# Kernel tuning notes

Measured on AMD Instinct MI355X. Metric: run time of the kernel, lower is better.

## Reference

```python
import jax, jax.numpy as jnp
import numpy as np

T, WQ, WS, C, H, W = 2, 75, 25, 640, 10, 10
WAY, SHOT = 5, 5
HID = C // 16
SCALE_VALUE = 30.0
ATTEN_SCALE_VALUE = 50.0
FROM_VALUE = 0.5
VALUE_INTERVAL = 0.3
BN_EPS = 1e-5
NORM_EPS = 1e-12


def _leaky(x):
    return jnp.where(x >= 0, x, 0.2 * x)


def _l2norm(x, axis):
    n = jnp.sqrt(jnp.sum(x * x, axis=axis, keepdims=True))
    return x / jnp.maximum(n, NORM_EPS)


def _embed(x, W_conv, bn_gamma, bn_beta, bn_mean, bn_var):
    # 1x1 conv (no bias) + eval-mode BatchNorm + LeakyReLU(0.2)
    # x: [t, n, c, h, w] -> [t, n, c, h, w]
    y = jnp.einsum('oc,tnchw->tnohw', W_conv, x)
    inv = bn_gamma / jnp.sqrt(bn_var + BN_EPS)
    y = y * inv[:, None, None] + (bn_beta - bn_mean * inv)[:, None, None]
    return _leaky(y)


def setup_inputs() -> dict:
    key = jax.random.key(0)
    ks = jax.random.split(key, 5)
    return {
        'query_feat': jax.random.normal(ks[0], (T, WQ, C, H, W), dtype=jnp.float32),
        'support_feat': jax.random.normal(ks[1], (T, WS, C, H, W), dtype=jnp.float32),
        'W_conv': jax.random.normal(ks[2], (C, C), dtype=jnp.float32) * 0.02,
        'bn_gamma': jnp.ones((C,), jnp.float32),
        'bn_beta': jnp.zeros((C,), jnp.float32),
        'bn_mean': jnp.zeros((C,), jnp.float32),
        'bn_var': jnp.ones((C,), jnp.float32),
        'psi_w1': jax.random.normal(ks[3], (C, HID), dtype=jnp.float32) * 0.04,
        'psi_b1': jnp.zeros((HID,), jnp.float32),
        'psi_w2': jax.random.normal(ks[4], (HID, 1), dtype=jnp.float32) * 0.15,
        'psi_b2': jnp.zeros((1,), jnp.float32),
        'way_num': WAY,
        'shot_num': SHOT,
    }


def reference(query_feat, support_feat, W_conv, bn_gamma, bn_beta, bn_mean, bn_var,
              psi_w1, psi_b1, psi_w2, psi_b2, way_num, shot_num):
    t, wq, c, h, w = query_feat.shape
    ws = support_feat.shape[1]
    hw = h * w

    # embedded + normalized features for the gated branch
    w_query = _embed(query_feat, W_conv, bn_gamma, bn_beta, bn_mean, bn_var)
    w_query = w_query.reshape(t, wq, c, hw).transpose(0, 1, 3, 2)      # [t, wq, hw, c]
    w_support = _embed(support_feat, W_conv, bn_gamma, bn_beta, bn_mean, bn_var)
    w_support = w_support.reshape(t, ws, c, hw).transpose(0, 2, 1, 3).reshape(t, c, ws * hw)
    w_query = _l2norm(w_query, axis=3)
    w_support = _l2norm(w_support, axis=1)

    # cosine similarity of embedded features: [t, wq, hw, ws*hw]
    f_x = jnp.einsum('tqpc,tck->tqpk', w_query, w_support)

    # AEAModule: per-location adaptive threshold from f_psi MLP
    hid = _leaky(w_query @ psi_w1 + psi_b1)                            # [t, wq, hw, HID]
    clamp_value = jax.nn.sigmoid(hid @ psi_w2 + psi_b2) * VALUE_INTERVAL + FROM_VALUE
    clamp_fx = jax.nn.sigmoid(ATTEN_SCALE_VALUE * (f_x - clamp_value))
    atten_score = clamp_fx / jnp.maximum(
        jnp.sum(jnp.abs(clamp_fx), axis=-1, keepdims=True), NORM_EPS)  # L1 normalize

    # raw-feature cosine similarity
    qf = _l2norm(query_feat.reshape(t, wq, c, hw).transpose(0, 1, 3, 2), axis=3)
    sf = _l2norm(support_feat.reshape(t, ws, c, hw).transpose(0, 2, 1, 3).reshape(t, c, ws * hw), axis=1)
    match_score = jnp.einsum('tqpc,tck->tqpk', qf, sf)                 # [t, wq, hw, ws*hw]

    # gate, regroup support axis into (way, shot, hw_s), reduce
    ams = (atten_score * match_score).reshape(t, wq, hw, way_num, shot_num, hw)
    score = ams.sum(axis=-1).mean(axis=(2, 4)) * SCALE_VALUE           # [t, wq, way]
    return score
```

## Files before the change

### kernel.cpp

```cpp
#include <hip/hip_runtime.h>
#include <stdint.h>

#define T_    2
#define WQ_   75
#define WS_   25
#define C_    640
#define HW_   100
#define HID_  40
#define WAY_  5
#define QP_   (WQ_*HW_)
#define SP_   (WS_*HW_)
#define QPAD_ 128
#define KPAD_ 512
#define KROWS_ (WAY_*KPAD_)
#define C8_   (C_/8)
#define BM_   256
#define QSTR_ (C8_*QPAD_*8)

typedef _Float16 f16;
typedef _Float16 f16x8 __attribute__((ext_vector_type(8)));
typedef _Float16 f16x4 __attribute__((ext_vector_type(4)));
typedef _Float16 f16x16 __attribute__((ext_vector_type(16)));
typedef float    f32x4 __attribute__((ext_vector_type(4)));
typedef float    f32x16 __attribute__((ext_vector_type(16)));
typedef uint32_t u32;

__device__ __forceinline__ void gl_lds16(const f16* g, f16* l) {
  __builtin_amdgcn_global_load_lds(
      (const __attribute__((address_space(1))) u32*)g,
      (__attribute__((address_space(3))) u32*)l, 16, 0, 0);
}

__global__ __launch_bounds__(128) void k0_invnorm(
    const float* __restrict__ q, const float* __restrict__ s,
    float* __restrict__ rq_inv, float* __restrict__ rq_nrm,
    float* __restrict__ rs_inv, float* __restrict__ rs_nrm) {
  int b = blockIdx.x;
  int t = b / (WQ_ + WS_);
  int n = b % (WQ_ + WS_);
  int p = threadIdx.x;
  if (p >= HW_) return;
  const float* base; float* oi; float* on; int idx;
  if (n < WQ_) {
    base = q + ((size_t)(t*WQ_ + n))*C_*HW_;
    idx = t*QP_ + n*HW_ + p; oi = rq_inv; on = rq_nrm;
  } else {
    int m = n - WQ_;
    base = s + ((size_t)(t*WS_ + m))*C_*HW_;
    idx = t*SP_ + m*HW_ + p; oi = rs_inv; on = rs_nrm;
  }
  float ss = 0.f;
  for (int c = 0; c < C_; ++c) { float v = base[c*HW_ + p]; ss += v*v; }
  float nrm = fmaxf(sqrtf(ss), 1e-12f);
  oi[idx] = 1.f/nrm; on[idx] = nrm;
}

__global__ __launch_bounds__(256) void kw_packW(
    const float* __restrict__ W, const float* __restrict__ w1,
    f16* __restrict__ Wr, f16* __restrict__ Wt8, f16* __restrict__ w1t) {
  int idx = blockIdx.x*256 + threadIdx.x;
  if (idx < C_*C8_) {
    int o = idx / C8_, c8 = idx % C8_;
    f16x8 v;
#pragma unroll
    for (int i = 0; i < 8; ++i) v[i] = (f16)W[(size_t)o*C_ + c8*8 + i];
    *reinterpret_cast<f16x8*>(Wr + (size_t)o*C_ + c8*8) = v;
    *reinterpret_cast<f16x8*>(Wt8 + ((size_t)c8*C_ + o)*8) = v;
  } else if (idx < C_*C8_ + 48*C8_) {
    int k2 = idx - C_*C8_;
    int h = k2 / C8_, c8 = k2 % C8_;
    f16x8 v;
#pragma unroll
    for (int i = 0; i < 8; ++i)
      v[i] = (h < HID_) ? (f16)w1[(size_t)(c8*8+i)*HID_ + h] : (f16)0.f;
    *reinterpret_cast<f16x8*>(w1t + (size_t)h*C_ + c8*8) = v;
  }
}

__global__ __launch_bounds__(256) void k1_pack_qraw(
    const float* __restrict__ q, const float* __restrict__ rq_inv,
    f16* __restrict__ Bq_raw) {
  int b = blockIdx.x;
  int ct = b % 10; b /= 10;
  int qq = b % WQ_; int t = b / WQ_;
  int c0 = ct*64;
  size_t tq = (size_t)t*WQ_ + qq;
  __shared__ float lds[64*HW_];
  const float4* s4 = reinterpret_cast<const float4*>(
      q + ((tq)*C_ + c0)*HW_);
  float4* l4 = reinterpret_cast<float4*>(lds);
  for (int i = threadIdx.x; i < 64*HW_/4; i += 256) l4[i] = s4[i];
  __syncthreads();
  for (int ch = threadIdx.x; ch < 8*QPAD_; ch += 256) {
    int lc8 = ch / QPAD_, p = ch % QPAD_;
    float inv = (p < HW_) ? rq_inv[t*QP_ + qq*HW_ + p] : 0.f;
    f16x8 v;
#pragma unroll
    for (int i = 0; i < 8; ++i) {
      float x = (p < HW_) ? lds[(lc8*8 + i)*HW_ + p] : 0.f;
      v[i] = (f16)(x * inv);
    }
    *reinterpret_cast<f16x8*>(Bq_raw + (tq*C8_ + c0/8 + lc8)*((size_t)QPAD_*8) + (size_t)p*8) = v;
  }
}

__global__ __launch_bounds__(256) void k2_pack_sraw(
    const float* __restrict__ s, const float* __restrict__ rs_inv,
    f16* __restrict__ As_raw) {
  int b = blockIdx.x;
  int ct = b % 10; b /= 10;
  int n = b % WS_; int t = b / WS_;
  int c0 = ct*64;
  __shared__ float lds[64*HW_];
  const float4* s4 = reinterpret_cast<const float4*>(
      s + (((size_t)(t*WS_ + n))*C_ + c0)*HW_);
  float4* l4 = reinterpret_cast<float4*>(lds);
  for (int i = threadIdx.x; i < 64*HW_/4; i += 256) l4[i] = s4[i];
  __syncthreads();
  for (int ch = threadIdx.x; ch < HW_*8; ch += 256) {
    int p = ch / 8, cc = ch % 8;
    float inv = rs_inv[t*SP_ + n*HW_ + p];
    f16x8 v;
#pragma unroll
    for (int i = 0; i < 8; ++i) v[i] = (f16)(lds[(cc*8 + i)*HW_ + p] * inv);
    int k = n*HW_ + p;
    int way = k / 500, ki = k % 500;
    size_t row = (size_t)t*KROWS_ + way*KPAD_ + ki;
    *reinterpret_cast<f16x8*>(As_raw + row*C_ + c0 + cc*8) = v;
  }
}

__global__ __launch_bounds__(512) void k3_embed_support(
    const f16* __restrict__ As_raw, const f16* __restrict__ Wt8,
    const float* __restrict__ rs_nrm,
    const float* __restrict__ g, const float* __restrict__ be,
    const float* __restrict__ mu, const float* __restrict__ va,
    f16* __restrict__ As_emb) {
  int b = blockIdx.x;
  int t = b / (KROWS_/64);
  int row0 = (b % (KROWS_/64)) * 64;
  int tid = threadIdx.x, wv = tid >> 6, lane = tid & 63;
  int mf = wv & 3, nh = wv >> 2;
  __shared__ f16 Alds[64*32];
  __shared__ f16 Blds[32*C_];
  __shared__ float rowss[64];
  f32x4 acc[20];
#pragma unroll
  for (int i = 0; i < 20; ++i) acc[i] = (f32x4){0.f,0.f,0.f,0.f};

  for (int cs = 0; cs < 20; ++cs) {
    int c0 = cs*32;
    if (tid < 256) {
      int r = tid >> 2, ch = tid & 3;
      *reinterpret_cast<f16x8*>(Alds + r*32 + ch*8) =
        *reinterpret_cast<const f16x8*>(As_raw + ((size_t)t*KROWS_ + row0 + r)*C_ + c0 + ch*8);
    }
    const f16x8* bsrc = reinterpret_cast<const f16x8*>(Wt8 + (size_t)(c0/8)*C_*8);
    f16x8* bdst = reinterpret_cast<f16x8*>(Blds);
    for (int i = tid; i < 4*C_; i += 512) bdst[i] = bsrc[i];
    __syncthreads();
    f16x8 a = *reinterpret_cast<const f16x8*>(Alds + (mf*16 + (lane&15))*32 + (lane>>4)*8);
#pragma unroll
    for (int nf = 0; nf < 20; ++nf) {
      int o = nh*320 + nf*16 + (lane & 15);
      f16x8 bf = *reinterpret_cast<const f16x8*>(Blds + (((lane>>4)*C_) + o)*8);
      acc[nf] = __builtin_amdgcn_mfma_f32_16x16x32_f16(a, bf, acc[nf], 0, 0, 0);
    }
    __syncthreads();
  }

  if (tid < 64) rowss[tid] = 0.f;
  __syncthreads();
  int rg = lane >> 4, cl = lane & 15;
  int prow = row0 + mf*16 + rg*4;
#pragma unroll
  for (int j = 0; j < 4; ++j) {
    int pr = prow + j;
    int way = pr / KPAD_, ki = pr - way*KPAD_;
    bool valid = ki < 500;
    float nrm = valid ? rs_nrm[t*SP_ + way*500 + ki] : 0.f;
    float ssum = 0.f;
#pragma unroll
    for (int nf = 0; nf < 20; ++nf) {
      int o = nh*320 + nf*16 + cl;
      float inv = g[o] / sqrtf(va[o] + 1e-5f);
      float sh = be[o] - mu[o]*inv;
      float y = acc[nf][j]*nrm*inv + sh;
      y = (y >= 0.f) ? y : 0.2f*y;
      if (!valid) y = 0.f;
      acc[nf][j] = y;
      ssum += y*y;
    }
#pragma unroll
    for (int m = 1; m < 16; m <<= 1) ssum += __shfl_xor(ssum, m);
    if (cl == 0) atomicAdd(&rowss[mf*16 + rg*4 + j], ssum);
  }
  __syncthreads();
#pragma unroll
  for (int j = 0; j < 4; ++j) {
    int pr = prow + j;
    int ki = pr - (pr / KPAD_)*KPAD_;
    if (ki >= 500) continue;
    float invn = 1.f / fmaxf(sqrtf(rowss[mf*16 + rg*4 + j]), 1e-12f);
#pragma unroll
    for (int nf = 0; nf < 20; ++nf) {
      int o = nh*320 + nf*16 + cl;
      As_emb[((size_t)t*KROWS_ + pr)*C_ + o] = (f16)(acc[nf][j]*invn);
    }
  }
}

__global__ __launch_bounds__(256, 3) void k4_embed_query(
    const f16* __restrict__ Wr, const f16* __restrict__ Bq_raw,
    const float* __restrict__ rq_nrm,
    const float* __restrict__ g, const float* __restrict__ be,
    const float* __restrict__ mu, const float* __restrict__ va,
    f16* __restrict__ Bq_emb) {
  __shared__ f16 Ab[3][128*32];
  __shared__ f16 Bb[3][4*QPAD_*8];
  int b = blockIdx.x;
  int ot = b % 5; b /= 5;
  int qq = b % WQ_; int t = b / WQ_;
  int o0 = ot*128;
  size_t tq = (size_t)t*WQ_ + qq;
  int tid = threadIdx.x, w = tid >> 6, lane = tid & 63;
  int la_r = lane >> 2, la_c = lane & 3;

  auto stage = [&](int buf, int cs) {
#pragma unroll
    for (int i = 0; i < 2; ++i) {
      int ca = w*2 + i;
      int r = ca*16 + la_r;
      int sc = la_c ^ (r & 3);
      gl_lds16(Wr + (size_t)(o0 + r)*C_ + cs*32 + sc*8, &Ab[buf][ca*512]);
    }
#pragma unroll
    for (int i = 0; i < 2; ++i) {
      int cb = w*2 + i;
      int c8l = cb >> 1;
      size_t src = (tq*C8_ + cs*4 + c8l)*(size_t)(QPAD_*8) + (size_t)((cb&1)*64 + lane)*8;
      gl_lds16(Bq_raw + src, &Bb[buf][(c8l*QPAD_ + (cb&1)*64)*8]);
    }
  };

  f32x4 acc[2][8];
#pragma unroll
  for (int a = 0; a < 2; ++a)
#pragma unroll
    for (int n = 0; n < 8; ++n) acc[a][n] = (f32x4){0.f,0.f,0.f,0.f};

  stage(0, 0);
  stage(1, 1);
  for (int cs = 0; cs < 20; ++cs) {
    int buf = cs % 3;
    if (cs < 19) asm volatile("s_waitcnt vmcnt(4)" ::: "memory");
    else         asm volatile("s_waitcnt vmcnt(0)" ::: "memory");
    __builtin_amdgcn_s_barrier();
    if (cs < 18) stage((cs+2)%3, cs+2);
    __builtin_amdgcn_s_setprio(1);
    f16x8 fa[2];
#pragma unroll
    for (int mi = 0; mi < 2; ++mi) {
      int R = w*32 + mi*16 + (lane & 15);
      int sc = (lane >> 4) ^ (R & 3);
      fa[mi] = *reinterpret_cast<const f16x8*>(&Ab[buf][R*32 + sc*8]);
    }
#pragma unroll
    for (int nf = 0; nf < 8; ++nf) {
      f16x8 fb = *reinterpret_cast<const f16x8*>(
          &Bb[buf][((lane>>4)*QPAD_ + nf*16 + (lane&15))*8]);
#pragma unroll
      for (int mi = 0; mi < 2; ++mi)
        acc[mi][nf] = __builtin_amdgcn_mfma_f32_16x16x32_f16(fa[mi], fb, acc[mi][nf], 0, 0, 0);
    }
    __builtin_amdgcn_s_setprio(0);
  }

#pragma unroll
  for (int mi = 0; mi < 2; ++mi) {
    int obase = o0 + w*32 + mi*16 + (lane>>4)*4;
    float inv4[4], sh4[4];
#pragma unroll
    for (int j = 0; j < 4; ++j) {
      int o = obase + j;
      inv4[j] = g[o] / sqrtf(va[o] + 1e-5f);
      sh4[j] = be[o] - mu[o]*inv4[j];
    }
#pragma unroll
    for (int nf = 0; nf < 8; ++nf) {
      int pp = nf*16 + (lane & 15);
      float nrmv = (pp < HW_) ? rq_nrm[t*QP_ + qq*HW_ + pp] : 0.f;
      f16x4 vv;
#pragma unroll
      for (int j = 0; j < 4; ++j) {
        float y = (pp < HW_) ? (acc[mi][nf][j]*nrmv*inv4[j] + sh4[j]) : 0.f;
        y = (y >= 0.f) ? y : 0.2f*y;
        vv[j] = (f16)y;
      }
      *reinterpret_cast<f16x4*>(
          &Bq_emb[(tq*C8_ + (obase>>3))*((size_t)QPAD_*8) + (size_t)pp*8 + (obase&7)]) = vv;
    }
  }
}

__global__ __launch_bounds__(256) void k5_colnorm_psi(
    f16* __restrict__ Bq_emb, const f16* __restrict__ w1t,
    const float* __restrict__ b1, const float* __restrict__ w2,
    const float* __restrict__ b2, float* __restrict__ cv) {
  __shared__ float ssA[2][QPAD_];
  __shared__ float invs[QPAD_];
  __shared__ float hidL[48*QPAD_];
  int bq = blockIdx.x;
  int tid = threadIdx.x, w = tid >> 6, lane = tid & 63;
  size_t base = (size_t)bq * QSTR_;

  {
    int h2 = tid >> 7, pp = tid & 127;
    float ss = 0.f;
    for (int c8 = h2*40; c8 < h2*40 + 40; ++c8) {
      f16x8 v = *reinterpret_cast<const f16x8*>(&Bq_emb[base + ((size_t)c8*QPAD_ + pp)*8]);
#pragma unroll
      for (int i = 0; i < 8; ++i) { float x = (float)v[i]; ss += x*x; }
    }
    ssA[h2][pp] = ss;
  }
  for (int i = tid; i < 48*QPAD_; i += 256) hidL[i] = 0.f;
  __syncthreads();
  if (tid < QPAD_) invs[tid] = 1.f / fmaxf(sqrtf(ssA[0][tid] + ssA[1][tid]), 1e-12f);

  f32x4 acc[3][8];
#pragma unroll
  for (int a = 0; a < 3; ++a)
#pragma unroll
    for (int n = 0; n < 8; ++n) acc[a][n] = (f32x4){0.f,0.f,0.f,0.f};
  for (int r = 0; r < 5; ++r) {
    int cs = w + r*4;
    f16x8 fa[3];
#pragma unroll
    for (int mf = 0; mf < 3; ++mf) {
      int R = mf*16 + (lane & 15);
      fa[mf] = *reinterpret_cast<const f16x8*>(&w1t[(size_t)R*C_ + cs*32 + (lane>>4)*8]);
    }
#pragma unroll
    for (int nf = 0; nf < 8; ++nf) {
      f16x8 fb = *reinterpret_cast<const f16x8*>(
          &Bq_emb[base + ((size_t)(cs*4 + (lane>>4))*QPAD_ + nf*16 + (lane&15))*8]);
#pragma unroll
      for (int mf = 0; mf < 3; ++mf)
        acc[mf][nf] = __builtin_amdgcn_mfma_f32_16x16x32_f16(fa[mf], fb, acc[mf][nf], 0, 0, 0);
    }
  }
  __syncthreads();
  for (int rr = 0; rr < 4; ++rr) {
    if (w == rr) {
#pragma unroll
      for (int mf = 0; mf < 3; ++mf)
#pragma unroll
        for (int nf = 0; nf < 8; ++nf)
#pragma unroll
          for (int j = 0; j < 4; ++j) {
            int row = mf*16 + (lane>>4)*4 + j;
            int col = nf*16 + (lane & 15);
            hidL[row*QPAD_ + col] += acc[mf][nf][j];
          }
    }
    __syncthreads();
  }
  if (tid < QPAD_) {
    float inv = invs[tid];
    float z = b2[0];
    for (int h = 0; h < HID_; ++h) {
      float hv = hidL[h*QPAD_ + tid]*inv + b1[h];
      hv = (hv >= 0.f) ? hv : 0.2f*hv;
      z += hv*w2[h];
    }
    cv[bq*QPAD_ + tid] = 0.3f/(1.f + __expf(-z)) + 0.5f;
  }
  for (int i = tid; i < C8_*QPAD_; i += 256) {
    int pp = i & 127;
    f16* ptr = Bq_emb + base + (size_t)i*8;
    f16x8 v = *reinterpret_cast<const f16x8*>(ptr);
    float inv = invs[pp];
    f16x8 o;
#pragma unroll
    for (int j = 0; j < 8; ++j) o[j] = (f16)((float)v[j]*inv);
    *reinterpret_cast<f16x8*>(ptr) = o;
  }
}

__global__ __launch_bounds__(256, 2) void k6_main(
    const f16* __restrict__ As_emb, const f16* __restrict__ As_raw,
    const f16* __restrict__ Bq_emb, const f16* __restrict__ Bq_raw,
    const float* __restrict__ cv,
    float* __restrict__ Spart, float* __restrict__ L1part) {
  __shared__ f16 Ab[3][BM_*32];
  __shared__ f16 Bb[3][4*QPAD_*8];
  __shared__ float cvs[QPAD_], Ss[QPAD_], L1s[QPAD_];

  int bid = blockIdx.x;
  int xcd = bid & 7, j0 = bid >> 3;
  int l = (xcd < 4) ? xcd*188 + j0 : 752 + (xcd-4)*187 + j0;
  int kt = l & 1; int m = l >> 1;
  int q = m % WQ_; int gidx = m / WQ_;
  int t = gidx / WAY_, way = gidx - t*WAY_;

  int tid = threadIdx.x, w = tid >> 6, lane = tid & 63;
  size_t tq = (size_t)t*WQ_ + q;
  if (tid < QPAD_) {
    cvs[tid] = cv[tq*QPAD_ + tid];
    Ss[tid] = 0.f; L1s[tid] = 0.f;
  }
  int wrow0 = w*64;
  int la_r = lane >> 2, la_c = lane & 3;
  size_t Arowbase = (size_t)t*KROWS_ + (size_t)way*KPAD_ + (size_t)kt*BM_;

  auto stage = [&](int buf, int ph) {
    int pass = ph / 20, cs = ph - pass*20;
    const f16* As = (pass == 0) ? As_raw : As_emb;
    const f16* Bs = (pass == 0) ? Bq_raw : Bq_emb;
#pragma unroll
    for (int i = 0; i < 4; ++i) {
      int ca = w*4 + i;
      int r = ca*16 + la_r;
      int sc = la_c ^ (r & 3);
      gl_lds16(As + (Arowbase + r)*C_ + cs*32 + sc*8, &Ab[buf][ca*512]);
    }
#pragma unroll
    for (int i = 0; i < 2; ++i) {
      int cb = w*2 + i;
      int c8l = cb >> 1;
      size_t src = (tq*C8_ + cs*4 + c8l)*(size_t)(QPAD_*8) + (size_t)((cb&1)*64 + lane)*8;
      gl_lds16(Bs + src, &Bb[buf][(c8l*QPAD_ + (cb&1)*64)*8]);
    }
  };

  f32x16 acc[2][4];
  f16x16 mtc[2][4];
#pragma unroll
  for (int mi = 0; mi < 2; ++mi)
#pragma unroll
    for (int nf = 0; nf < 4; ++nf) acc[mi][nf] = (f32x16)(0.f);
  float Sl[4] = {0,0,0,0}, L1l[4] = {0,0,0,0};

  stage(0, 0);
  stage(1, 1);

  for (int ph = 0; ph < 40; ++ph) {
    int buf = ph % 3;
    if (ph < 39) asm volatile("s_waitcnt vmcnt(6)" ::: "memory");
    else         asm volatile("s_waitcnt vmcnt(0)" ::: "memory");
    __builtin_amdgcn_s_barrier();
    if (ph < 38) stage((ph+2)%3, ph+2);
    __builtin_amdgcn_s_setprio(1);
    const f16* Abuf = Ab[buf];
    const f16* Bbuf = Bb[buf];
    int r0 = wrow0 + (lane & 31);
    int r1 = r0 + 32;
    int rsw = r0 & 3;
#pragma unroll
    for (int ks = 0; ks < 2; ++ks) {
      int c8l = ks*2 + (lane >> 5);
      int pc = c8l ^ rsw;
      f16x8 fa0 = *reinterpret_cast<const f16x8*>(&Abuf[r0*32 + pc*8]);
      f16x8 fa1 = *reinterpret_cast<const f16x8*>(&Abuf[r1*32 + pc*8]);
#pragma unroll
      for (int nf = 0; nf < 4; ++nf) {
        f16x8 fb = *reinterpret_cast<const f16x8*>(
            &Bbuf[(c8l*QPAD_ + nf*32 + (lane & 31))*8]);
        acc[0][nf] = __builtin_amdgcn_mfma_f32_32x32x16_f16(fa0, fb, acc[0][nf], 0, 0, 0);
        acc[1][nf] = __builtin_amdgcn_mfma_f32_32x32x16_f16(fa1, fb, acc[1][nf], 0, 0, 0);
      }
    }
    __builtin_amdgcn_s_setprio(0);

    if (ph == 19) {
#pragma unroll
      for (int mi = 0; mi < 2; ++mi)
#pragma unroll
        for (int nf = 0; nf < 4; ++nf) {
#pragma unroll
          for (int jj = 0; jj < 16; ++jj) {
            mtc[mi][nf][jj] = (f16)acc[mi][nf][jj];
            acc[mi][nf][jj] = 0.f;
          }
        }
    } else if (ph == 39) {
#pragma unroll
      for (int mi = 0; mi < 2; ++mi)
#pragma unroll
        for (int nf = 0; nf < 4; ++nf) {
          float cvv = cvs[nf*32 + (lane & 31)];
#pragma unroll
          for (int jj = 0; jj < 16; ++jj) {
            float sg = 1.f/(1.f + __expf(-50.f*(acc[mi][nf][jj] - cvv)));
            Sl[nf]  += sg * (float)mtc[mi][nf][jj];
            L1l[nf] += sg;
          }
        }
    }
  }

#pragma unroll
  for (int nf = 0; nf < 4; ++nf) {
    float vs = Sl[nf] + __shfl_xor(Sl[nf], 32);
    float vl = L1l[nf] + __shfl_xor(L1l[nf], 32);
    if (lane < 32) {
      atomicAdd(&Ss[nf*32 + lane], vs);
      atomicAdd(&L1s[nf*32 + lane], vl);
    }
  }
  __syncthreads();
  if (tid < QPAD_) {
    size_t o = ((tq*WAY_ + way)*2 + kt)*(size_t)QPAD_ + tid;
    Spart[o] = Ss[tid]; L1part[o] = L1s[tid];
  }
}

__global__ __launch_bounds__(128) void k7_reduce(
    const float* __restrict__ Spart, const float* __restrict__ L1part,
    float* __restrict__ out) {
  int b = blockIdx.x;
  int tid = threadIdx.x;
  __shared__ float red[128];
  float contrib[WAY_] = {0,0,0,0,0};
  if (tid < HW_) {
    size_t base = (size_t)b*WAY_*2*QPAD_;
    float l1 = 0.f;
#pragma unroll
    for (int w = 0; w < WAY_; ++w)
#pragma unroll
      for (int k = 0; k < 2; ++k) l1 += L1part[base + (w*2+k)*QPAD_ + tid];
    l1 = fmaxf(l1, 1e-12f);
#pragma unroll
    for (int w = 0; w < WAY_; ++w)
      contrib[w] = (Spart[base + (w*2+0)*QPAD_ + tid] +
                    Spart[base + (w*2+1)*QPAD_ + tid]) / l1;
  }
#pragma unroll
  for (int w = 0; w < WAY_; ++w) {
    red[tid] = contrib[w];
    __syncthreads();
    for (int off = 64; off > 0; off >>= 1) {
      if (tid < off) red[tid] += red[tid + off];
      __syncthreads();
    }
    if (tid == 0) out[b*WAY_ + w] = red[0] * 30.f / (float)(HW_*5);
    __syncthreads();
  }
}

extern "C" void kernel_launch(void* const* d_in, const int* in_sizes, int n_in,
                              void* d_out, int out_size, void* d_ws, size_t ws_size,
                              hipStream_t stream) {
  (void)in_sizes; (void)n_in; (void)out_size; (void)ws_size;
  const float* q  = (const float*)d_in[0];
  const float* s  = (const float*)d_in[1];
  const float* W  = (const float*)d_in[2];
  const float* g  = (const float*)d_in[3];
  const float* be = (const float*)d_in[4];
  const float* mu = (const float*)d_in[5];
  const float* va = (const float*)d_in[6];
  const float* w1 = (const float*)d_in[7];
  const float* b1 = (const float*)d_in[8];
  const float* w2 = (const float*)d_in[9];
  const float* b2 = (const float*)d_in[10];
  float* out = (float*)d_out;
  char* ws = (char*)d_ws;

  size_t off = 0;
  auto nxt = [&](size_t bytes) { size_t o = off; off += (bytes + 255) & ~(size_t)255; return o; };
  float* rq_inv = (float*)(ws + nxt((size_t)T_*QP_*4));
  float* rq_nrm = (float*)(ws + nxt((size_t)T_*QP_*4));
  float* rs_inv = (float*)(ws + nxt((size_t)T_*SP_*4));
  float* rs_nrm = (float*)(ws + nxt((size_t)T_*SP_*4));
  f16* Wr     = (f16*)(ws + nxt((size_t)C_*C_*2));
  f16* Wt8    = (f16*)(ws + nxt((size_t)C_*C_*2));
  f16* w1t    = (f16*)(ws + nxt((size_t)48*C_*2));
  f16* As_raw = (f16*)(ws + nxt((size_t)T_*KROWS_*C_*2));
  f16* As_emb = (f16*)(ws + nxt((size_t)T_*KROWS_*C_*2));
  f16* Bq_raw = (f16*)(ws + nxt((size_t)T_*WQ_*QSTR_*2));
  f16* Bq_emb = (f16*)(ws + nxt((size_t)T_*WQ_*QSTR_*2));
  float* cvp    = (float*)(ws + nxt((size_t)T_*WQ_*QPAD_*4));
  float* Spart  = (float*)(ws + nxt((size_t)T_*WQ_*WAY_*2*QPAD_*4));
  float* L1part = (float*)(ws + nxt((size_t)T_*WQ_*WAY_*2*QPAD_*4));

  hipMemsetAsync(As_raw, 0, (size_t)T_*KROWS_*C_*2, stream);
  hipMemsetAsync(As_emb, 0, (size_t)T_*KROWS_*C_*2, stream);

  k0_invnorm<<<T_*(WQ_+WS_), 128, 0, stream>>>(q, s, rq_inv, rq_nrm, rs_inv, rs_nrm);
  kw_packW<<<(C_*C8_ + 48*C8_ + 255)/256, 256, 0, stream>>>(W, w1, Wr, Wt8, w1t);
  k1_pack_qraw<<<T_*WQ_*10, 256, 0, stream>>>(q, rq_inv, Bq_raw);
  k2_pack_sraw<<<T_*WS_*10, 256, 0, stream>>>(s, rs_inv, As_raw);
  k3_embed_support<<<T_*(KROWS_/64), 512, 0, stream>>>(As_raw, Wt8, rs_nrm, g, be, mu, va, As_emb);
  k4_embed_query<<<T_*WQ_*5, 256, 0, stream>>>(Wr, Bq_raw, rq_nrm, g, be, mu, va, Bq_emb);
  k5_colnorm_psi<<<T_*WQ_, 256, 0, stream>>>(Bq_emb, w1t, b1, w2, b2, cvp);
  k6_main<<<1500, 256, 0, stream>>>(As_emb, As_raw, Bq_emb, Bq_raw, cvp, Spart, L1part);
  k7_reduce<<<T_*WQ_, 128, 0, stream>>>(Spart, L1part, out);
}
```

Before: 337.3 us.

## Re-layout support matrices channel-blocked, defer query normalization, split k0 reduction

The support raw and embedded matrices are stored channel-group-major ([c8][row][8]), so each k6 stage becomes a few contiguous 16-byte global-to-LDS loads with simple pointer increments instead of swizzled per-row loads. The in-place rescale pass over Bq_emb in k5 is dropped; the per-query inverse norm is stored and applied to the accumulator inside k6's epilogue. k0 now spreads its channel reduction over 512 threads with an LDS combine. The match-score f16 cache is clamped to [-8, 8] before conversion, and the unswizzled LDS layout may add bank conflicts.

```diff
diff --git a/kernel.cpp b/kernel.cpp
--- a/kernel.cpp
+++ b/kernel.cpp
@@ -31,15 +31,16 @@
       (__attribute__((address_space(3))) u32*)l, 16, 0, 0);
 }
 
-__global__ __launch_bounds__(128) void k0_invnorm(
+__global__ __launch_bounds__(512) void k0_invnorm(
     const float* __restrict__ q, const float* __restrict__ s,
     float* __restrict__ rq_inv, float* __restrict__ rq_nrm,
     float* __restrict__ rs_inv, float* __restrict__ rs_nrm) {
+  __shared__ float part[4][128];
   int b = blockIdx.x;
   int t = b / (WQ_ + WS_);
   int n = b % (WQ_ + WS_);
-  int p = threadIdx.x;
-  if (p >= HW_) return;
+  int tid = threadIdx.x;
+  int seg = tid >> 7, p = tid & 127;
   const float* base; float* oi; float* on; int idx;
   if (n < WQ_) {
     base = q + ((size_t)(t*WQ_ + n))*C_*HW_;
@@ -50,9 +51,18 @@
     idx = t*SP_ + m*HW_ + p; oi = rs_inv; on = rs_nrm;
   }
   float ss = 0.f;
-  for (int c = 0; c < C_; ++c) { float v = base[c*HW_ + p]; ss += v*v; }
-  float nrm = fmaxf(sqrtf(ss), 1e-12f);
-  oi[idx] = 1.f/nrm; on[idx] = nrm;
+  if (p < HW_) {
+    for (int c = seg*160; c < seg*160 + 160; ++c) {
+      float v = base[c*HW_ + p]; ss += v*v;
+    }
+  }
+  part[seg][p] = ss;
+  __syncthreads();
+  if (seg == 0 && p < HW_) {
+    float tot = part[0][p] + part[1][p] + part[2][p] + part[3][p];
+    float nrm = fmaxf(sqrtf(tot), 1e-12f);
+    oi[idx] = 1.f/nrm; on[idx] = nrm;
+  }
 }
 
 __global__ __launch_bounds__(256) void kw_packW(
@@ -125,8 +135,8 @@
     for (int i = 0; i < 8; ++i) v[i] = (f16)(lds[(cc*8 + i)*HW_ + p] * inv);
     int k = n*HW_ + p;
     int way = k / 500, ki = k % 500;
-    size_t row = (size_t)t*KROWS_ + way*KPAD_ + ki;
-    *reinterpret_cast<f16x8*>(As_raw + row*C_ + c0 + cc*8) = v;
+    size_t row = (size_t)way*KPAD_ + ki;
+    *reinterpret_cast<f16x8*>(As_raw + ((size_t)(t*C8_ + c0/8 + cc)*KROWS_ + row)*8) = v;
   }
 }
 
@@ -149,17 +159,18 @@
   for (int i = 0; i < 20; ++i) acc[i] = (f32x4){0.f,0.f,0.f,0.f};
 
   for (int cs = 0; cs < 20; ++cs) {
-    int c0 = cs*32;
     if (tid < 256) {
-      int r = tid >> 2, ch = tid & 3;
-      *reinterpret_cast<f16x8*>(Alds + r*32 + ch*8) =
-        *reinterpret_cast<const f16x8*>(As_raw + ((size_t)t*KROWS_ + row0 + r)*C_ + c0 + ch*8);
-    }
-    const f16x8* bsrc = reinterpret_cast<const f16x8*>(Wt8 + (size_t)(c0/8)*C_*8);
+      int c8l = tid >> 6, r = tid & 63;
+      *reinterpret_cast<f16x8*>(Alds + (c8l*64 + r)*8) =
+        *reinterpret_cast<const f16x8*>(
+            As_raw + ((size_t)(t*C8_ + cs*4 + c8l)*KROWS_ + row0 + r)*8);
+    }
+    const f16x8* bsrc = reinterpret_cast<const f16x8*>(Wt8 + (size_t)(cs*4)*C_*8);
     f16x8* bdst = reinterpret_cast<f16x8*>(Blds);
     for (int i = tid; i < 4*C_; i += 512) bdst[i] = bsrc[i];
     __syncthreads();
-    f16x8 a = *reinterpret_cast<const f16x8*>(Alds + (mf*16 + (lane&15))*32 + (lane>>4)*8);
+    f16x8 a = *reinterpret_cast<const f16x8*>(
+        Alds + ((lane>>4)*64 + mf*16 + (lane&15))*8);
 #pragma unroll
     for (int nf = 0; nf < 20; ++nf) {
       int o = nh*320 + nf*16 + (lane & 15);
@@ -205,7 +216,7 @@
 #pragma unroll
     for (int nf = 0; nf < 20; ++nf) {
       int o = nh*320 + nf*16 + cl;
-      As_emb[((size_t)t*KROWS_ + pr)*C_ + o] = (f16)(acc[nf][j]*invn);
+      As_emb[((size_t)(t*C8_ + (o>>3))*KROWS_ + pr)*8 + (o&7)] = (f16)(acc[nf][j]*invn);
     }
   }
 }
@@ -304,9 +315,10 @@
 }
 
 __global__ __launch_bounds__(256) void k5_colnorm_psi(
-    f16* __restrict__ Bq_emb, const f16* __restrict__ w1t,
+    const f16* __restrict__ Bq_emb, const f16* __restrict__ w1t,
     const float* __restrict__ b1, const float* __restrict__ w2,
-    const float* __restrict__ b2, float* __restrict__ cv) {
+    const float* __restrict__ b2, float* __restrict__ cv,
+    float* __restrict__ invq) {
   __shared__ float ssA[2][QPAD_];
   __shared__ float invs[QPAD_];
   __shared__ float hidL[48*QPAD_];
@@ -326,7 +338,12 @@
   }
   for (int i = tid; i < 48*QPAD_; i += 256) hidL[i] = 0.f;
   __syncthreads();
-  if (tid < QPAD_) invs[tid] = 1.f / fmaxf(sqrtf(ssA[0][tid] + ssA[1][tid]), 1e-12f);
+  if (tid < QPAD_) {
+    float ss = ssA[0][tid] + ssA[1][tid];
+    float inv = (ss > 0.f) ? (1.f / fmaxf(sqrtf(ss), 1e-12f)) : 0.f;
+    invs[tid] = inv;
+    invq[bq*QPAD_ + tid] = inv;
+  }
 
   f32x4 acc[3][8];
 #pragma unroll
@@ -376,26 +393,16 @@
     }
     cv[bq*QPAD_ + tid] = 0.3f/(1.f + __expf(-z)) + 0.5f;
   }
-  for (int i = tid; i < C8_*QPAD_; i += 256) {
-    int pp = i & 127;
-    f16* ptr = Bq_emb + base + (size_t)i*8;
-    f16x8 v = *reinterpret_cast<const f16x8*>(ptr);
-    float inv = invs[pp];
-    f16x8 o;
-#pragma unroll
-    for (int j = 0; j < 8; ++j) o[j] = (f16)((float)v[j]*inv);
-    *reinterpret_cast<f16x8*>(ptr) = o;
-  }
 }
 
 __global__ __launch_bounds__(256, 2) void k6_main(
     const f16* __restrict__ As_emb, const f16* __restrict__ As_raw,
     const f16* __restrict__ Bq_emb, const f16* __restrict__ Bq_raw,
-    const float* __restrict__ cv,
+    const float* __restrict__ cv, const float* __restrict__ invq,
     float* __restrict__ Spart, float* __restrict__ L1part) {
-  __shared__ f16 Ab[3][BM_*32];
+  __shared__ f16 Ab[3][4*BM_*8];
   __shared__ f16 Bb[3][4*QPAD_*8];
-  __shared__ float cvs[QPAD_], Ss[QPAD_], L1s[QPAD_];
+  __shared__ float cvs[QPAD_], iqs[QPAD_], Ss[QPAD_], L1s[QPAD_];
 
   int bid = blockIdx.x;
   int xcd = bid & 7, j0 = bid >> 3;
@@ -408,30 +415,30 @@
   size_t tq = (size_t)t*WQ_ + q;
   if (tid < QPAD_) {
     cvs[tid] = cv[tq*QPAD_ + tid];
+    iqs[tid] = invq[tq*QPAD_ + tid];
     Ss[tid] = 0.f; L1s[tid] = 0.f;
   }
   int wrow0 = w*64;
-  int la_r = lane >> 2, la_c = lane & 3;
-  size_t Arowbase = (size_t)t*KROWS_ + (size_t)way*KPAD_ + (size_t)kt*BM_;
-
-  auto stage = [&](int buf, int ph) {
-    int pass = ph / 20, cs = ph - pass*20;
-    const f16* As = (pass == 0) ? As_raw : As_emb;
-    const f16* Bs = (pass == 0) ? Bq_raw : Bq_emb;
-#pragma unroll
-    for (int i = 0; i < 4; ++i) {
-      int ca = w*4 + i;
-      int r = ca*16 + la_r;
-      int sc = la_c ^ (r & 3);
-      gl_lds16(As + (Arowbase + r)*C_ + cs*32 + sc*8, &Ab[buf][ca*512]);
-    }
-#pragma unroll
-    for (int i = 0; i < 2; ++i) {
-      int cb = w*2 + i;
-      int c8l = cb >> 1;
-      size_t src = (tq*C8_ + cs*4 + c8l)*(size_t)(QPAD_*8) + (size_t)((cb&1)*64 + lane)*8;
-      gl_lds16(Bs + src, &Bb[buf][(c8l*QPAD_ + (cb&1)*64)*8]);
-    }
+  size_t rowb = (size_t)way*KPAD_ + (size_t)kt*BM_;
+
+  const size_t aoff = ((size_t)(t*C8_ + w)*KROWS_ + rowb + lane)*8;
+  const size_t boff = ((tq*C8_ + w)*(size_t)QPAD_ + lane)*8;
+  const f16* pA = As_raw + aoff;
+  const f16* pB = Bq_raw + boff;
+  const f16* pA1 = As_emb + aoff;
+  const f16* pB1 = Bq_emb + boff;
+  const int CS_A = 4*KROWS_*8;
+  const int CS_B = 4*QPAD_*8;
+
+  auto stage = [&](int buf, const f16* a, const f16* bsrc) {
+    f16* da = &Ab[buf][(size_t)w*BM_*8];
+    f16* db = &Bb[buf][(size_t)w*QPAD_*8];
+    gl_lds16(a,        da);
+    gl_lds16(a + 512,  da + 512);
+    gl_lds16(a + 1024, da + 1024);
+    gl_lds16(a + 1536, da + 1536);
+    gl_lds16(bsrc,       db);
+    gl_lds16(bsrc + 512, db + 512);
   };
 
   f32x16 acc[2][4];
@@ -442,27 +449,25 @@
     for (int nf = 0; nf < 4; ++nf) acc[mi][nf] = (f32x16)(0.f);
   float Sl[4] = {0,0,0,0}, L1l[4] = {0,0,0,0};
 
-  stage(0, 0);
-  stage(1, 1);
+  stage(0, pA, pB); pA += CS_A; pB += CS_B;
+  stage(1, pA, pB); pA += CS_A; pB += CS_B;
 
   for (int ph = 0; ph < 40; ++ph) {
+    if (ph == 18) { pA = pA1; pB = pB1; }
     int buf = ph % 3;
     if (ph < 39) asm volatile("s_waitcnt vmcnt(6)" ::: "memory");
     else         asm volatile("s_waitcnt vmcnt(0)" ::: "memory");
     __builtin_amdgcn_s_barrier();
-    if (ph < 38) stage((ph+2)%3, ph+2);
+    if (ph < 38) { stage((ph+2)%3, pA, pB); pA += CS_A; pB += CS_B; }
     __builtin_amdgcn_s_setprio(1);
     const f16* Abuf = Ab[buf];
     const f16* Bbuf = Bb[buf];
     int r0 = wrow0 + (lane & 31);
-    int r1 = r0 + 32;
-    int rsw = r0 & 3;
 #pragma unroll
     for (int ks = 0; ks < 2; ++ks) {
       int c8l = ks*2 + (lane >> 5);
-      int pc = c8l ^ rsw;
-      f16x8 fa0 = *reinterpret_cast<const f16x8*>(&Abuf[r0*32 + pc*8]);
-      f16x8 fa1 = *reinterpret_cast<const f16x8*>(&Abuf[r1*32 + pc*8]);
+      f16x8 fa0 = *reinterpret_cast<const f16x8*>(&Abuf[(c8l*BM_ + r0)*8]);
+      f16x8 fa1 = *reinterpret_cast<const f16x8*>(&Abuf[(c8l*BM_ + r0 + 32)*8]);
 #pragma unroll
       for (int nf = 0; nf < 4; ++nf) {
         f16x8 fb = *reinterpret_cast<const f16x8*>(
@@ -480,23 +485,26 @@
         for (int nf = 0; nf < 4; ++nf) {
 #pragma unroll
           for (int jj = 0; jj < 16; ++jj) {
-            mtc[mi][nf][jj] = (f16)acc[mi][nf][jj];
+            mtc[mi][nf][jj] = (f16)fminf(fmaxf(acc[mi][nf][jj], -8.f), 8.f);
             acc[mi][nf][jj] = 0.f;
           }
         }
     } else if (ph == 39) {
 #pragma unroll
-      for (int mi = 0; mi < 2; ++mi)
-#pragma unroll
-        for (int nf = 0; nf < 4; ++nf) {
-          float cvv = cvs[nf*32 + (lane & 31)];
+      for (int nf = 0; nf < 4; ++nf) {
+        int col = nf*32 + (lane & 31);
+        float cvv = cvs[col];
+        float iq = iqs[col];
+#pragma unroll
+        for (int mi = 0; mi < 2; ++mi)
 #pragma unroll
           for (int jj = 0; jj < 16; ++jj) {
-            float sg = 1.f/(1.f + __expf(-50.f*(acc[mi][nf][jj] - cvv)));
+            float fx = acc[mi][nf][jj] * iq;
+            float sg = 1.f/(1.f + __expf(-50.f*(fx - cvv)));
             Sl[nf]  += sg * (float)mtc[mi][nf][jj];
             L1l[nf] += sg;
           }
-        }
+      }
     }
   }
 
@@ -581,19 +589,20 @@
   f16* Bq_raw = (f16*)(ws + nxt((size_t)T_*WQ_*QSTR_*2));
   f16* Bq_emb = (f16*)(ws + nxt((size_t)T_*WQ_*QSTR_*2));
   float* cvp    = (float*)(ws + nxt((size_t)T_*WQ_*QPAD_*4));
+  float* invq   = (float*)(ws + nxt((size_t)T_*WQ_*QPAD_*4));
   float* Spart  = (float*)(ws + nxt((size_t)T_*WQ_*WAY_*2*QPAD_*4));
   float* L1part = (float*)(ws + nxt((size_t)T_*WQ_*WAY_*2*QPAD_*4));
 
   hipMemsetAsync(As_raw, 0, (size_t)T_*KROWS_*C_*2, stream);
   hipMemsetAsync(As_emb, 0, (size_t)T_*KROWS_*C_*2, stream);
 
-  k0_invnorm<<<T_*(WQ_+WS_), 128, 0, stream>>>(q, s, rq_inv, rq_nrm, rs_inv, rs_nrm);
+  k0_invnorm<<<T_*(WQ_+WS_), 512, 0, stream>>>(q, s, rq_inv, rq_nrm, rs_inv, rs_nrm);
   kw_packW<<<(C_*C8_ + 48*C8_ + 255)/256, 256, 0, stream>>>(W, w1, Wr, Wt8, w1t);
   k1_pack_qraw<<<T_*WQ_*10, 256, 0, stream>>>(q, rq_inv, Bq_raw);
   k2_pack_sraw<<<T_*WS_*10, 256, 0, stream>>>(s, rs_inv, As_raw);
   k3_embed_support<<<T_*(KROWS_/64), 512, 0, stream>>>(As_raw, Wt8, rs_nrm, g, be, mu, va, As_emb);
   k4_embed_query<<<T_*WQ_*5, 256, 0, stream>>>(Wr, Bq_raw, rq_nrm, g, be, mu, va, Bq_emb);
-  k5_colnorm_psi<<<T_*WQ_, 256, 0, stream>>>(Bq_emb, w1t, b1, w2, b2, cvp);
-  k6_main<<<1500, 256, 0, stream>>>(As_emb, As_raw, Bq_emb, Bq_raw, cvp, Spart, L1part);
+  k5_colnorm_psi<<<T_*WQ_, 256, 0, stream>>>(Bq_emb, w1t, b1, w2, b2, cvp, invq);
+  k6_main<<<1500, 256, 0, stream>>>(As_emb, As_raw, Bq_emb, Bq_raw, cvp, invq, Spart, L1part);
   k7_reduce<<<T_*WQ_, 128, 0, stream>>>(Spart, L1part, out);
 }
```

After: 311.6 us. -7.6%, faster.
